# Performance work log

Measured on AMD Instinct MI355X. Metric: run time of the kernel, lower is better.

Reference implementation:

```python
import jax, jax.numpy as jnp
import numpy as np

B, T, P, H, D = 2, 2048, 1024, 16, 128
C = H * D  # 2048
ROPE_THETA = 10000.0


def setup_inputs() -> dict:
    key = jax.random.key(0)
    ks = jax.random.split(key, 5)
    x = jax.random.normal(ks[0], (B, T, C), jnp.float32)
    w_qkv = jax.random.normal(ks[1], (C, 3 * C), jnp.float32) * 0.02  # Linear(dim, 3*dim), applied as x @ w
    w_out = jax.random.normal(ks[2], (C, C), jnp.float32) * 0.02
    past_k = jax.random.normal(ks[3], (B, H, P, D), jnp.float32)
    past_v = jax.random.normal(ks[4], (B, H, P, D), jnp.float32)
    return {"x": x, "w_qkv": w_qkv, "w_out": w_out, "past_k": past_k, "past_v": past_v}


def _rope(q, k, offset):
    # rotate-half RoPE (GPT-NeoX style), positions offset..offset+T-1
    d = q.shape[-1]
    inv_freq = 1.0 / (ROPE_THETA ** (jnp.arange(0, d, 2, dtype=jnp.float32) / d))  # [d/2]
    pos = offset + jnp.arange(q.shape[2], dtype=jnp.float32)                        # [T]
    ang = pos[:, None] * inv_freq[None, :]                                          # [T, d/2]
    cos = jnp.concatenate([jnp.cos(ang), jnp.cos(ang)], -1)[None, None]             # [1,1,T,d]
    sin = jnp.concatenate([jnp.sin(ang), jnp.sin(ang)], -1)[None, None]

    def rot_half(t):
        t1, t2 = jnp.split(t, 2, axis=-1)
        return jnp.concatenate([-t2, t1], -1)

    return q * cos + rot_half(q) * sin, k * cos + rot_half(k) * sin


def reference(x, w_qkv, w_out, past_k, past_v):
    Bv, Tv, Cv = x.shape
    Hn = past_k.shape[1]
    Dd = Cv // Hn
    # fused QKV projection
    qkv = x @ w_qkv                       # [B,T,3C]
    q, k, v = jnp.split(qkv, 3, axis=-1)  # each [B,T,C]

    def split_heads(t):
        return t.reshape(Bv, Tv, Hn, Dd).transpose(0, 2, 1, 3)  # [B,H,T,D]

    q, k, v = split_heads(q), split_heads(k), split_heads(v)
    # RoPE with offset = past length
    q, k = _rope(q, k, past_k.shape[2])
    # KV-cache concat along time axis
    k = jnp.concatenate([past_k, k], axis=2)  # [B,H,P+T,D]
    v = jnp.concatenate([past_v, v], axis=2)
    # SDPA: past_kv present -> is_causal=False, no mask (full attention)
    scale = 1.0 / jnp.sqrt(jnp.float32(Dd))
    scores = jnp.einsum('bhqd,bhkd->bhqk', q, k) * scale
    attn = jax.nn.softmax(scores, axis=-1)
    out = jnp.einsum('bhqk,bhkd->bhqd', attn, v)
    out = out.transpose(0, 2, 1, 3).reshape(Bv, Tv, Cv)
    return out @ w_out
```

## Files before the change

kernel.cpp:

```cpp
#include <hip/hip_runtime.h>
#include <stdint.h>

#define B_ 2
#define T_ 2048
#define P_ 1024
#define H_ 16
#define D_ 128
#define C_ 2048
#define S_ 3072
#define M_ 4096
#define N3_ 6144

typedef unsigned short u16;
typedef unsigned int uint32;
typedef __attribute__((ext_vector_type(8))) short short8;
typedef __attribute__((ext_vector_type(8))) __bf16 bf16x8;
typedef __attribute__((ext_vector_type(4))) float f32x4;
typedef __attribute__((ext_vector_type(16))) float f32x16;
typedef __attribute__((ext_vector_type(4))) unsigned short u16x4;
typedef __attribute__((ext_vector_type(4))) unsigned int uint4v;

static __device__ __forceinline__ float bf2f(u16 h) {
    union { unsigned int u; float f; } x; x.u = ((unsigned int)h) << 16; return x.f;
}
static __device__ __forceinline__ u16 f2bf(float f) {
    return __builtin_bit_cast(u16, (__bf16)f);
}
static __device__ __forceinline__ uint32 cvtpk(float lo, float hi) {
    uint32 r;
    asm("v_cvt_pk_bf16_f32 %0, %1, %2" : "=v"(r) : "v"(lo), "v"(hi));
    return r;
}
#define MAX3(a, b, c) fmaxf(fmaxf((a), (b)), (c))

static __device__ __forceinline__ f32x4 mfma_bf16(short8 a, short8 b, f32x4 c) {
    return __builtin_amdgcn_mfma_f32_16x16x32_bf16(
        __builtin_bit_cast(bf16x8, a), __builtin_bit_cast(bf16x8, b), c, 0, 0, 0);
}
static __device__ __forceinline__ f32x16 mfma32(short8 a, short8 b, f32x16 c) {
    return __builtin_amdgcn_mfma_f32_32x32x16_bf16(
        __builtin_bit_cast(bf16x8, a), __builtin_bit_cast(bf16x8, b), c, 0, 0, 0);
}

typedef __attribute__((address_space(3))) unsigned int lds_u32;
typedef const __attribute__((address_space(1))) unsigned int glb_u32;
static __device__ __forceinline__ void gload_lds16(const void* g, void* l) {
    __builtin_amdgcn_global_load_lds((glb_u32*)g, (lds_u32*)l, 16, 0, 0);
}

static __device__ __forceinline__ void storeC(float* p, float v) { *p = v; }
static __device__ __forceinline__ void storeC(u16* p, float v) { *p = f2bf(v); }


__global__ void castx_kernel(const float* __restrict__ x, u16* __restrict__ Xb) {
    int idx = blockIdx.x * 256 + threadIdx.x;
    const float4 v = ((const float4*)x)[idx];
    u16x4 o;
    o.x = f2bf(v.x); o.y = f2bf(v.y); o.z = f2bf(v.z); o.w = f2bf(v.w);
    ((u16x4*)Xb)[idx] = o;
}

__global__ void wT_kernel(const float* __restrict__ W, u16* __restrict__ Wt,
                          int Ndim, int Kdim) {
    __shared__ float tile[64][65];
    const int n0 = blockIdx.x * 64, k0 = blockIdx.y * 64;
    const int tid = threadIdx.x;
#pragma unroll
    for (int i = 0; i < 16; i++) {
        int idx = tid + i * 256;
        int r = idx >> 6, c = idx & 63;
        tile[r][c] = W[(size_t)(k0 + r) * Ndim + n0 + c];
    }
    __syncthreads();
#pragma unroll
    for (int i = 0; i < 16; i++) {
        int idx = tid + i * 256;
        int r = idx >> 6, c = idx & 63;
        Wt[(size_t)(n0 + r) * Kdim + k0 + c] = f2bf(tile[c][r]);
    }
}

__global__ void rope_table_kernel(float* __restrict__ cosT, float* __restrict__ sinT) {
    int idx = blockIdx.x * 256 + threadIdx.x;
    int t = idx >> 6, d = idx & 63;
    float inv = powf(10000.0f, -(float)d * (1.0f / 64.0f));
    float ang = (float)(P_ + t) * inv;
    cosT[idx] = cosf(ang);
    sinT[idx] = sinf(ang);
}

__global__ void rope_qk_kernel(u16* __restrict__ QKVb, u16* __restrict__ Kc,
                               const float* __restrict__ cosT,
                               const float* __restrict__ sinT) {
    int idx = blockIdx.x * 256 + threadIdx.x;
    int d = idx & 63;
    int h = (idx >> 6) & 15;
    int t = (idx >> 10) & 2047;
    int b = idx >> 21;
    size_t rowoff = (size_t)(b * T_ + t) * N3_;
    float c = cosT[(t << 6) + d], s = sinT[(t << 6) + d];
    {
        u16* p1 = QKVb + rowoff + h * 128 + d;
        float x1 = bf2f(p1[0]), x2 = bf2f(p1[64]);
        p1[0]  = f2bf(x1 * c - x2 * s);
        p1[64] = f2bf(x2 * c + x1 * s);
    }
    {
        const u16* p1 = QKVb + rowoff + C_ + h * 128 + d;
        float x1 = bf2f(p1[0]), x2 = bf2f(p1[64]);
        u16* o = Kc + ((size_t)(b * H_ + h) * S_ + P_ + t) * 128 + d;
        o[0]  = f2bf(x1 * c - x2 * s);
        o[64] = f2bf(x2 * c + x1 * s);
    }
}

__global__ void pastk_kernel(const float* __restrict__ past_k, u16* __restrict__ Kc) {
    int idx = blockIdx.x * 256 + threadIdx.x;
    int d = idx & 127;
    int p = (idx >> 7) & 1023;
    int bh = idx >> 17;
    Kc[((size_t)bh * S_ + p) * 128 + d] = f2bf(past_k[idx]);
}

__global__ void vnewT_kernel(const u16* __restrict__ QKVb, u16* __restrict__ Vt) {
    __shared__ u16 tile[64][65];
    const int t0 = blockIdx.x * 64, d0 = blockIdx.y * 64, bh = blockIdx.z;
    const int b = bh >> 4, h = bh & 15;
    const int tid = threadIdx.x;
#pragma unroll
    for (int i = 0; i < 16; i++) {
        int idx = tid + i * 256;
        int r = idx >> 6, c = idx & 63;
        tile[r][c] = QKVb[(size_t)(b * T_ + t0 + r) * N3_ + 2 * C_ + h * 128 + d0 + c];
    }
    __syncthreads();
#pragma unroll
    for (int i = 0; i < 16; i++) {
        int idx = tid + i * 256;
        int r = idx >> 6, c = idx & 63;
        Vt[((size_t)bh * 128 + d0 + r) * S_ + P_ + t0 + c] = tile[c][r];
    }
}

__global__ void vpastT_kernel(const float* __restrict__ past_v, u16* __restrict__ Vt) {
    __shared__ float tile[64][65];
    const int p0 = blockIdx.x * 64, d0 = blockIdx.y * 64, bh = blockIdx.z;
    const int tid = threadIdx.x;
#pragma unroll
    for (int i = 0; i < 16; i++) {
        int idx = tid + i * 256;
        int r = idx >> 6, c = idx & 63;
        tile[r][c] = past_v[((size_t)bh * P_ + p0 + r) * 128 + d0 + c];
    }
    __syncthreads();
#pragma unroll
    for (int i = 0; i < 16; i++) {
        int idx = tid + i * 256;
        int r = idx >> 6, c = idx & 63;
        Vt[((size_t)bh * 128 + d0 + r) * S_ + p0 + c] = f2bf(tile[c][r]);
    }
}

template <typename OutT>
__global__ void __launch_bounds__(512, 1)
gemm3(const u16* __restrict__ A, const u16* __restrict__ Bt,
      OutT* __restrict__ Co, int Mdim, int Ndim, int Kdim) {
    __shared__ u16 lA[3 * 256 * 64];
    __shared__ u16 lB[3 * 128 * 64];
    const int nbx = Ndim >> 7;
    const int nwg = (Mdim >> 8) * nbx;
    int bid = blockIdx.x;
    int wg = (bid & 7) * (nwg >> 3) + (bid >> 3);
    const int bm = wg / nbx, bn = wg % nbx;
    const int m0 = bm << 8, n0 = bn << 7;
    const int tid = threadIdx.x;
    const int wave = tid >> 6, lane = tid & 63;
    const int mw = wave >> 1, nw = wave & 1;
    const int l15 = lane & 15, l4 = lane >> 4;

    f32x4 acc[4][4];
#pragma unroll
    for (int i = 0; i < 4; i++)
#pragma unroll
        for (int j = 0; j < 4; j++) acc[i][j] = (f32x4){0.f, 0.f, 0.f, 0.f};

    const u16* aSrc[4];
    const u16* bSrc[2];
#pragma unroll
    for (int i = 0; i < 4; i++) {
        int cid = i * 512 + tid;
        int r = cid >> 3, pc = cid & 7;
        aSrc[i] = A + (size_t)(m0 + r) * Kdim + ((pc ^ (r & 7)) << 3);
    }
#pragma unroll
    for (int i = 0; i < 2; i++) {
        int cid = i * 512 + tid;
        int r = cid >> 3, pc = cid & 7;
        bSrc[i] = Bt + (size_t)(n0 + r) * Kdim + ((pc ^ (r & 7)) << 3);
    }

#define STAGE3(bi, kt) do {                                                     \
    u16* _pa = lA + (bi) * 16384 + wave * 512;                                  \
    u16* _pb = lB + (bi) * 8192 + wave * 512;                                   \
    _Pragma("unroll")                                                           \
    for (int i = 0; i < 4; i++)                                                 \
        gload_lds16(aSrc[i] + (size_t)(kt) * 64, _pa + i * 4096);               \
    _Pragma("unroll")                                                           \
    for (int i = 0; i < 2; i++)                                                 \
        gload_lds16(bSrc[i] + (size_t)(kt) * 64, _pb + i * 4096);               \
} while (0)

    STAGE3(0, 0);
    STAGE3(1, 1);

    const int NT = Kdim >> 6;
    int bc = 0;
    for (int t = 0; t < NT; ++t) {
        if (t + 1 < NT) asm volatile("s_waitcnt vmcnt(6)" ::: "memory");
        else            asm volatile("s_waitcnt vmcnt(0)" ::: "memory");
        __builtin_amdgcn_s_barrier();
        asm volatile("" ::: "memory");
        if (t + 2 < NT) {
            int b2 = bc + 2; if (b2 >= 3) b2 -= 3;
            STAGE3(b2, t + 2);
        }
        const u16* la = lA + bc * 16384;
        const u16* lb = lB + bc * 8192;
        short8 af[4][2], bf[4][2];
#pragma unroll
        for (int i = 0; i < 4; i++)
#pragma unroll
            for (int kk = 0; kk < 2; kk++) {
                int r = mw * 64 + i * 16 + l15;
                int cb = (kk * 64 + l4 * 16) ^ ((r & 7) << 4);
                af[i][kk] = *(const short8*)&la[r * 64 + (cb >> 1)];
            }
#pragma unroll
        for (int j = 0; j < 4; j++)
#pragma unroll
            for (int kk = 0; kk < 2; kk++) {
                int r = nw * 64 + j * 16 + l15;
                int cb = (kk * 64 + l4 * 16) ^ ((r & 7) << 4);
                bf[j][kk] = *(const short8*)&lb[r * 64 + (cb >> 1)];
            }
        __builtin_amdgcn_s_setprio(1);
#pragma unroll
        for (int kk = 0; kk < 2; kk++)
#pragma unroll
            for (int i = 0; i < 4; i++)
#pragma unroll
                for (int j = 0; j < 4; j++)
                    acc[i][j] = mfma_bf16(af[i][kk], bf[j][kk], acc[i][j]);
        __builtin_amdgcn_s_setprio(0);
        __builtin_amdgcn_sched_barrier(0);
        bc = bc + 1; if (bc >= 3) bc = 0;
    }
#undef STAGE3

#pragma unroll
    for (int i = 0; i < 4; i++)
#pragma unroll
        for (int j = 0; j < 4; j++) {
            int row = m0 + mw * 64 + i * 16 + (l4 << 2);
            int col = n0 + nw * 64 + j * 16 + l15;
#pragma unroll
            for (int q = 0; q < 4; q++)
                storeC(&Co[(size_t)(row + q) * Ndim + col], acc[i][j][q]);
        }
}

__global__ void __launch_bounds__(256, 2)
attn_kernel(const u16* __restrict__ QKVb, const u16* __restrict__ Kc,
            const u16* __restrict__ Vt, u16* __restrict__ O) {
    __shared__ u16 ldsK[2][64 * 128];
    __shared__ u16 ldsV[2][128 * 64];

    int bid = blockIdx.x;
    int wg = (bid & 7) * 64 + (bid >> 3);
    const int qc = wg & 15;
    const int bh = wg >> 4;
    const int b = bh >> 4, h = bh & 15;
    const int tid = threadIdx.x, wave = tid >> 6, lane = tid & 63;
    const int l31 = lane & 31, hi = lane >> 5;

    const int krow = tid >> 4;
    const int kcol = (((tid & 15) << 4) ^ ((krow & 7) << 4)) >> 1;
    const int vrow = tid >> 3;
    const int vcol = (((tid & 7) << 4) ^ ((vrow & 7) << 4)) >> 1;

    const u16* Kbh = Kc + (size_t)bh * S_ * 128;
    const u16* Vbh = Vt + (size_t)bh * 128 * S_;

    const int tq = qc * 128 + wave * 32 + l31;
    short8 qf[8];
    {
        const u16* qp = QKVb + (size_t)(b * T_ + tq) * N3_ + h * 128 + hi * 8;
#pragma unroll
        for (int ks = 0; ks < 8; ks++) qf[ks] = *(const short8*)(qp + ks * 16);
    }

    f32x16 acco[4];
#pragma unroll
    for (int d = 0; d < 4; d++) acco[d] = (f32x16)(0.0f);
    float mrow = -1e30f, lrow = 0.f;
    const float sl2 = 0.08838834764831845f * 1.4426950408889634f;

#define STAGE(bufi, tt) do {                                                    \
    const int _s0 = (tt) * 64;                                                  \
    _Pragma("unroll")                                                           \
    for (int i = 0; i < 4; i++)                                                 \
        gload_lds16(Kbh + (size_t)(_s0 + krow + i * 16) * 128 + kcol,           \
                    (char*)&ldsK[bufi][0] + i * 4096 + wave * 1024);            \
    _Pragma("unroll")                                                           \
    for (int i = 0; i < 4; i++)                                                 \
        gload_lds16(Vbh + (size_t)(vrow + i * 32) * S_ + _s0 + vcol,            \
                    (char*)&ldsV[bufi][0] + i * 4096 + wave * 1024);            \
} while (0)

    STAGE(0, 0);
    __syncthreads();

    const int swz = (l31 & 7) << 4;

    for (int t = 0; t < S_ / 64; ++t) {
        const int cur = t & 1;
        if (t < S_ / 64 - 1) STAGE(cur ^ 1, t + 1);

        const u16* Kl = ldsK[cur];
        const u16* Vl = ldsV[cur];

        f32x16 p0 = (f32x16)(0.0f), p1 = (f32x16)(0.0f);
        __builtin_amdgcn_s_setprio(1);
#pragma unroll
        for (int ks = 0; ks < 8; ks++) {
            const int cidx = (((ks * 32 + hi * 16) ^ swz) >> 1);
            short8 k0 = *(const short8*)&Kl[(l31 << 7) + cidx];
            short8 k1 = *(const short8*)&Kl[((32 + l31) << 7) + cidx];
            p0 = mfma32(k0, qf[ks], p0);
            p1 = mfma32(k1, qf[ks], p1);
        }
        __builtin_amdgcn_s_setprio(0);

        float t0 = MAX3(p0[0], p0[1], p0[2]);
        float t1 = MAX3(p0[3], p0[4], p0[5]);
        float t2 = MAX3(p0[6], p0[7], p0[8]);
        float t3 = MAX3(p0[9], p0[10], p0[11]);
        float t4 = MAX3(p0[12], p0[13], p0[14]);
        float t5 = MAX3(p0[15], p1[0], p1[1]);
        float t6 = MAX3(p1[2], p1[3], p1[4]);
        float t7 = MAX3(p1[5], p1[6], p1[7]);
        float t8 = MAX3(p1[8], p1[9], p1[10]);
        float t9 = MAX3(p1[11], p1[12], p1[13]);
        float u0 = MAX3(t0, t1, t2);
        float u1 = MAX3(t3, t4, t5);
        float u2 = MAX3(t6, t7, t8);
        float u3 = MAX3(t9, p1[14], p1[15]);
        float pm = fmaxf(MAX3(u0, u1, u2), u3);
        pm = fmaxf(pm, __shfl_xor(pm, 32));
        float pmS = pm * sl2;
        if (!__all(pmS <= mrow + 8.0f)) {
            float mn = fmaxf(mrow, pmS);
            float fac = exp2f(mrow - mn);
            mrow = mn;
            lrow *= fac;
#pragma unroll
            for (int d = 0; d < 4; d++)
#pragma unroll
                for (int r = 0; r < 16; r++) acco[d][r] *= fac;
        }
        float s0a = 0.f, s1a = 0.f, s2a = 0.f, s3a = 0.f;
#pragma unroll
        for (int r = 0; r < 16; r += 4) {
            p0[r + 0] = exp2f(fmaf(p0[r + 0], sl2, -mrow)); s0a += p0[r + 0];
            p0[r + 1] = exp2f(fmaf(p0[r + 1], sl2, -mrow)); s1a += p0[r + 1];
            p0[r + 2] = exp2f(fmaf(p0[r + 2], sl2, -mrow)); s2a += p0[r + 2];
            p0[r + 3] = exp2f(fmaf(p0[r + 3], sl2, -mrow)); s3a += p0[r + 3];
        }
#pragma unroll
        for (int r = 0; r < 16; r += 4) {
            p1[r + 0] = exp2f(fmaf(p1[r + 0], sl2, -mrow)); s0a += p1[r + 0];
            p1[r + 1] = exp2f(fmaf(p1[r + 1], sl2, -mrow)); s1a += p1[r + 1];
            p1[r + 2] = exp2f(fmaf(p1[r + 2], sl2, -mrow)); s2a += p1[r + 2];
            p1[r + 3] = exp2f(fmaf(p1[r + 3], sl2, -mrow)); s3a += p1[r + 3];
        }
        float sum = (s0a + s1a) + (s2a + s3a);
        sum += __shfl_xor(sum, 32);
        lrow += sum;

        uint32 w[4][4];
#define PACK_HALF(pp, kh, ksout) do {                                           \
    uint32 A0 = cvtpk(pp[(kh)*8 + 0], pp[(kh)*8 + 1]);                          \
    uint32 A1 = cvtpk(pp[(kh)*8 + 2], pp[(kh)*8 + 3]);                          \
    uint32 B0 = cvtpk(pp[(kh)*8 + 4], pp[(kh)*8 + 5]);                          \
    uint32 B1 = cvtpk(pp[(kh)*8 + 6], pp[(kh)*8 + 7]);                          \
    uint32 sA0 = __shfl_xor(A0, 32), sA1 = __shfl_xor(A1, 32);                  \
    uint32 sB0 = __shfl_xor(B0, 32), sB1 = __shfl_xor(B1, 32);                  \
    w[ksout][0] = hi ? sB0 : A0;                                                \
    w[ksout][1] = hi ? sB1 : A1;                                                \
    w[ksout][2] = hi ? B0 : sA0;                                                \
    w[ksout][3] = hi ? B1 : sA1;                                                \
} while (0)
        PACK_HALF(p0, 0, 0);
        PACK_HALF(p0, 1, 1);
        PACK_HALF(p1, 0, 2);
        PACK_HALF(p1, 1, 3);
#undef PACK_HALF

        __builtin_amdgcn_s_setprio(1);
#pragma unroll
        for (int ks = 0; ks < 4; ks++) {
            uint4v pw = {w[ks][0], w[ks][1], w[ks][2], w[ks][3]};
            short8 pf = __builtin_bit_cast(short8, pw);
            const int cidx = (((ks * 32 + hi * 16) ^ swz) >> 1);
#pragma unroll
            for (int dblk = 0; dblk < 4; dblk++) {
                short8 vf = *(const short8*)&Vl[((dblk * 32 + l31) << 6) + cidx];
                acco[dblk] = mfma32(vf, pf, acco[dblk]);
            }
        }
        __builtin_amdgcn_s_setprio(0);

        __syncthreads();
    }
#undef STAGE

    float rl = 1.0f / lrow;
    u16* Op = O + (size_t)(b * T_ + tq) * C_ + h * 128;
#pragma unroll
    for (int dblk = 0; dblk < 4; dblk++)
#pragma unroll
        for (int j = 0; j < 4; j++) {
            u16x4 o;
            o.x = f2bf(acco[dblk][4 * j + 0] * rl);
            o.y = f2bf(acco[dblk][4 * j + 1] * rl);
            o.z = f2bf(acco[dblk][4 * j + 2] * rl);
            o.w = f2bf(acco[dblk][4 * j + 3] * rl);
            *(u16x4*)(Op + dblk * 32 + j * 8 + hi * 4) = o;
        }
}


extern "C" void kernel_launch(void* const* d_in, const int* in_sizes, int n_in,
                              void* d_out, int out_size, void* d_ws, size_t ws_size,
                              hipStream_t stream) {
    const float* x      = (const float*)d_in[0];
    const float* w_qkv  = (const float*)d_in[1];
    const float* w_out  = (const float*)d_in[2];
    const float* past_k = (const float*)d_in[3];
    const float* past_v = (const float*)d_in[4];
    float* out = (float*)d_out;

    char* ws = (char*)d_ws;
    u16* Xb    = (u16*)(ws);
    u16* Wqkvt = (u16*)(ws + 16777216);
    u16* Woutt = (u16*)(ws + 41943040);
    u16* QKVb  = (u16*)(ws + 50331648);
    u16* Kc    = (u16*)(ws + 100663296);
    u16* Vt    = (u16*)(ws + 125829120);
    u16* O     = (u16*)(ws + 150994944);
    float* cosT = (float*)(ws + 167772160);
    float* sinT = (float*)(ws + 168296448);

    castx_kernel<<<(M_ * C_ / 4) / 256, 256, 0, stream>>>(x, Xb);
    wT_kernel<<<dim3(N3_ / 64, C_ / 64), 256, 0, stream>>>(w_qkv, Wqkvt, N3_, C_);
    wT_kernel<<<dim3(C_ / 64, C_ / 64), 256, 0, stream>>>(w_out, Woutt, C_, C_);
    rope_table_kernel<<<(T_ * 64) / 256, 256, 0, stream>>>(cosT, sinT);

    gemm3<u16><<<(M_ / 256) * (N3_ / 128), 512, 0, stream>>>(Xb, Wqkvt, QKVb, M_, N3_, C_);

    rope_qk_kernel<<<(B_ * T_ * H_ * 64) / 256, 256, 0, stream>>>(QKVb, Kc, cosT, sinT);
    pastk_kernel<<<(B_ * H_ * P_ * D_) / 256, 256, 0, stream>>>(past_k, Kc);
    vnewT_kernel<<<dim3(T_ / 64, 2, B_ * H_), 256, 0, stream>>>(QKVb, Vt);
    vpastT_kernel<<<dim3(P_ / 64, 2, B_ * H_), 256, 0, stream>>>(past_v, Vt);

    attn_kernel<<<512, 256, 0, stream>>>(QKVb, Kc, Vt, O);

    gemm3<float><<<(M_ / 256) * (C_ / 128), 512, 0, stream>>>(O, Woutt, out, M_, C_, C_);
}
```

Baseline: 383.2 us.

## Interleave GEMM global prefetch and LDS reads with MFMA in four phases

Splits each K-tile iteration of the GEMM main loop into four phases, one per A row-block. Each phase loads its A fragments from LDS and issues part of the next-next tile's global-to-LDS prefetch, with B fragments loaded only in the first phase. The aim is to spread memory traffic across the MFMA work so LDS reads and global loads overlap compute more evenly. In exchange it adds two workgroup barriers per phase, eight per iteration, which may cost more than the overlap gains.

```diff
diff --git a/kernel.cpp b/kernel.cpp
--- a/kernel.cpp
+++ b/kernel.cpp
@@ -210,6 +210,17 @@
         gload_lds16(bSrc[i] + (size_t)(kt) * 64, _pb + i * 4096);               \
 } while (0)
 
+#define STAGE_A2(bi, kt, i0) do {                                               \
+    u16* _pa = lA + (bi) * 16384 + wave * 512;                                  \
+    gload_lds16(aSrc[i0] + (size_t)(kt) * 64, _pa + (i0) * 4096);               \
+    gload_lds16(aSrc[(i0) + 1] + (size_t)(kt) * 64, _pa + ((i0) + 1) * 4096);   \
+} while (0)
+#define STAGE_B2(bi, kt) do {                                                   \
+    u16* _pb = lB + (bi) * 8192 + wave * 512;                                   \
+    gload_lds16(bSrc[0] + (size_t)(kt) * 64, _pb);                              \
+    gload_lds16(bSrc[1] + (size_t)(kt) * 64, _pb + 4096);                       \
+} while (0)
+
     STAGE3(0, 0);
     STAGE3(1, 1);
 
@@ -220,42 +231,53 @@
         else            asm volatile("s_waitcnt vmcnt(0)" ::: "memory");
         __builtin_amdgcn_s_barrier();
         asm volatile("" ::: "memory");
-        if (t + 2 < NT) {
-            int b2 = bc + 2; if (b2 >= 3) b2 -= 3;
-            STAGE3(b2, t + 2);
-        }
+        int b2 = bc + 2; if (b2 >= 3) b2 -= 3;
+        const bool doStage = (t + 2 < NT);
         const u16* la = lA + bc * 16384;
         const u16* lb = lB + bc * 8192;
-        short8 af[4][2], bf[4][2];
-#pragma unroll
-        for (int i = 0; i < 4; i++)
+        short8 bf[4][2];
+#pragma unroll
+        for (int p = 0; p < 4; p++) {
+            short8 af2[2];
 #pragma unroll
             for (int kk = 0; kk < 2; kk++) {
-                int r = mw * 64 + i * 16 + l15;
+                int r = mw * 64 + p * 16 + l15;
                 int cb = (kk * 64 + l4 * 16) ^ ((r & 7) << 4);
-                af[i][kk] = *(const short8*)&la[r * 64 + (cb >> 1)];
+                af2[kk] = *(const short8*)&la[r * 64 + (cb >> 1)];
             }
-#pragma unroll
-        for (int j = 0; j < 4; j++)
-#pragma unroll
-            for (int kk = 0; kk < 2; kk++) {
-                int r = nw * 64 + j * 16 + l15;
-                int cb = (kk * 64 + l4 * 16) ^ ((r & 7) << 4);
-                bf[j][kk] = *(const short8*)&lb[r * 64 + (cb >> 1)];
+            if (p == 0) {
+#pragma unroll
+                for (int j = 0; j < 4; j++)
+#pragma unroll
+                    for (int kk = 0; kk < 2; kk++) {
+                        int r = nw * 64 + j * 16 + l15;
+                        int cb = (kk * 64 + l4 * 16) ^ ((r & 7) << 4);
+                        bf[j][kk] = *(const short8*)&lb[r * 64 + (cb >> 1)];
+                    }
             }
-        __builtin_amdgcn_s_setprio(1);
-#pragma unroll
-        for (int kk = 0; kk < 2; kk++)
-#pragma unroll
-            for (int i = 0; i < 4; i++)
+            if (doStage) {
+                if (p == 0) STAGE_A2(b2, t + 2, 0);
+                else if (p == 1) STAGE_A2(b2, t + 2, 2);
+                else if (p == 2) STAGE_B2(b2, t + 2);
+            }
+            __builtin_amdgcn_s_barrier();
+            asm volatile("" ::: "memory");
+            __builtin_amdgcn_s_setprio(1);
+#pragma unroll
+            for (int kk = 0; kk < 2; kk++)
 #pragma unroll
                 for (int j = 0; j < 4; j++)
-                    acc[i][j] = mfma_bf16(af[i][kk], bf[j][kk], acc[i][j]);
-        __builtin_amdgcn_s_setprio(0);
-        __builtin_amdgcn_sched_barrier(0);
+                    acc[p][j] = mfma_bf16(af2[kk], bf[j][kk], acc[p][j]);
+            __builtin_amdgcn_s_setprio(0);
+            __builtin_amdgcn_sched_barrier(0);
+            __builtin_amdgcn_s_barrier();
+            asm volatile("" ::: "memory");
+        }
         bc = bc + 1; if (bc >= 3) bc = 0;
     }
 #undef STAGE3
+#undef STAGE_A2
+#undef STAGE_B2
 
 #pragma unroll
     for (int i = 0; i < 4; i++)
```

After: 426.6 us. +11.3%, slower.
